# Kernel optimization log

Hardware: AMD Instinct MI355X
Metric: run time of the kernel (lower is better)

## Reference

```python
import math
import jax, jax.numpy as jnp
import numpy as np


def setup_inputs() -> dict:
    key = jax.random.key(0)
    k1, k2 = jax.random.split(key)
    x = jax.random.normal(k1, (32, 3, 64, 64), dtype=jnp.float32)   # (B,C,H,W)
    y = jax.random.normal(k2, (512, 3, 64, 64), dtype=jnp.float32)  # (N,C,H,W)
    return {"x": x, "y": y}


def reference(x, y):
    # Faithful to torch rfft/irfft with normalized=True (unitary / 'ortho' scaling).
    B, C, H, W = x.shape
    scale = math.sqrt(H * W)  # self.N in the torch module
    X = jnp.fft.rfft2(x, norm="ortho")  # (B,C,H,W//2+1) complex
    Y = jnp.fft.rfft2(y, norm="ortho")  # (N,C,H,W//2+1) complex
    # conj(X) . Y summed over channels, fused as one complex contraction
    G = jnp.einsum("bchw,nchw->bnhw", jnp.conj(X), Y)  # (B,N,H,W//2+1)
    g = jnp.fft.irfft2(G, s=(H, W), norm="ortho") * scale  # (B,N,H,W)
    m = jnp.max(g, axis=(-2, -1))  # MaxPool2d(kernel=input_size) -> (B,N)
    xx = jnp.linalg.norm(x.reshape(B, -1), axis=-1)[:, None]  # (B,1)
    yy = jnp.linalg.norm(y.reshape(y.shape[0], -1), axis=-1)[None, :]  # (1,N)
    return m / xx / yy
```

## Files before the change

### kernel.cpp

```cpp
#include <hip/hip_runtime.h>
#include <math.h>

#define FBINS 2112
#define CSC 66

typedef float cplx __attribute__((ext_vector_type(2)));
typedef __fp16 half2v __attribute__((ext_vector_type(2)));
#define MK2(a,b) (cplx){(float)(a), (float)(b)}

__device__ __forceinline__ cplx shufxy(cplx a){ return __builtin_shufflevector(a, a, 1, 0); }
template<int S> __device__ __forceinline__ cplx imul(cplx a){
    return (S > 0) ? shufxy(a) * MK2(-1.f, 1.f) : shufxy(a) * MK2(1.f, -1.f);
}
template<int S> __device__ __forceinline__ cplx cmul_tw(cplx a, cplx w){
    cplx ws = shufxy(w);
    return (S > 0) ? a.x*w + a.y*(ws*MK2(-1.f, 1.f))
                   : a.x*(w*MK2(1.f, -1.f)) + a.y*ws;
}

__device__ __forceinline__ unsigned pack16(float a, float b){
    half2v h = __builtin_amdgcn_cvt_pkrtz(a, b);
    return __builtin_bit_cast(unsigned, h);
}
__device__ __forceinline__ half2v h2(unsigned u){ return __builtin_bit_cast(half2v, u); }
__device__ __forceinline__ float fdot2(half2v a, half2v b, float c){
#if __has_builtin(__builtin_amdgcn_fdot2)
    return __builtin_amdgcn_fdot2(a, b, c, false);
#else
    return c + (float)a.x*(float)b.x + (float)a.y*(float)b.y;
#endif
}
__device__ __forceinline__ void dotw(unsigned ux, unsigned uy, float& r, float& s){
    unsigned ys = ((uy >> 16) | (uy << 16)) ^ 0x80000000u;
    r = fdot2(h2(ux), h2(uy), r);
    s = fdot2(h2(ux), h2(ys), s);
}
__device__ __forceinline__ void dotw_i(unsigned ux, unsigned uy, cplx& v){
    float rr = 0.f, ss = 0.f;
    dotw(ux, uy, rr, ss);
    v += MK2(-ss, rr);
}

__device__ __constant__ float TWC[112] = {
  1.f,0.f, 1.f,0.f, 1.f,0.f, 1.f,0.f, 1.f,0.f, 1.f,0.f, 1.f,0.f,
  0.9951847267f,0.0980171403f, 0.9807852804f,0.1950903220f, 0.9569403357f,0.2902846773f,
  0.9238795325f,0.3826834324f, 0.8819212643f,0.4713967368f, 0.8314696123f,0.5555702330f,
  0.7730104534f,0.6343932842f,
  0.9807852804f,0.1950903220f, 0.9238795325f,0.3826834324f, 0.8314696123f,0.5555702330f,
  0.7071067812f,0.7071067812f, 0.5555702330f,0.8314696123f, 0.3826834324f,0.9238795325f,
  0.1950903220f,0.9807852804f,
  0.9569403357f,0.2902846773f, 0.8314696123f,0.5555702330f, 0.6343932842f,0.7730104534f,
  0.3826834324f,0.9238795325f, 0.0980171403f,0.9951847267f, -0.1950903220f,0.9807852804f,
  -0.4713967368f,0.8819212643f,
  0.9238795325f,0.3826834324f, 0.7071067812f,0.7071067812f, 0.3826834324f,0.9238795325f,
  0.f,1.f, -0.3826834324f,0.9238795325f, -0.7071067812f,0.7071067812f,
  -0.9238795325f,0.3826834324f,
  0.8819212643f,0.4713967368f, 0.5555702330f,0.8314696123f, 0.0980171403f,0.9951847267f,
  -0.3826834324f,0.9238795325f, -0.7730104534f,0.6343932842f, -0.9807852804f,0.1950903220f,
  -0.9569403357f,-0.2902846773f,
  0.8314696123f,0.5555702330f, 0.3826834324f,0.9238795325f, -0.1950903220f,0.9807852804f,
  -0.7071067812f,0.7071067812f, -0.9807852804f,0.1950903220f, -0.9238795325f,-0.3826834324f,
  -0.5555702330f,-0.8314696123f,
  0.7730104534f,0.6343932842f, 0.1950903220f,0.9807852804f, -0.4713967368f,0.8819212643f,
  -0.9238795325f,0.3826834324f, -0.9569403357f,-0.2902846773f, -0.5555702330f,-0.8314696123f,
  0.0980171403f,-0.9951847267f
};
__device__ __forceinline__ void load_tw(int j, cplx wj[7]){
    #pragma unroll
    for (int k=0;k<7;++k) wj[k] = MK2(TWC[(j*7+k)*2], TWC[(j*7+k)*2+1]);
}

template<int S>
__device__ __forceinline__ void dft8(cplx v[8]) {
    const float C = 0.70710678118654752440f;
    cplx t0=v[0]+v[4], t4=v[0]-v[4];
    cplx t1=v[1]+v[5], t5=v[1]-v[5];
    cplx t2=v[2]+v[6], t6=v[2]-v[6];
    cplx t3=v[3]+v[7], t7=v[3]-v[7];
    cplx u0=t0+t2, u2=t0-t2;
    cplx u1=t1+t3, u3=t1-t3;
    v[0]=u0+u1; v[4]=u0-u1;
    cplx m3=imul<S>(u3);
    v[2]=u2+m3; v[6]=u2-m3;
    cplx z0=t4;
    cplx z1 = C*(t5 + imul<S>(t5));
    cplx z2 = imul<S>(t6);
    cplx z3 = C*(imul<S>(t7) - t7);
    cplx w0=z0+z2, w2=z0-z2;
    cplx w1=z1+z3, w3=z1-z3;
    v[1]=w0+w1; v[5]=w0-w1;
    cplx mb=imul<S>(w3);
    v[3]=w2+mb; v[7]=w2-mb;
}

template<int S>
__device__ __forceinline__ void fft64_from_regs(
    cplx v[8], cplx* __restrict__ mem, int base, int j, const cplx wj[7])
{
    dft8<S>(v);
    #pragma unroll
    for (int k=1;k<8;++k) v[k] = cmul_tw<S>(v[k], wj[k-1]);
    #pragma unroll
    for (int k=0;k<8;++k) mem[base + 8*j + (k^j)] = v[k];
    #pragma unroll
    for (int n=0;n<8;++n) v[n] = mem[base + 8*n + (j^n)];
    dft8<S>(v);
}

__global__ __launch_bounds__(256) void fwd_fft_kernel(
    const float* __restrict__ in, unsigned* __restrict__ o,
    float* __restrict__ pn)
{
    __shared__ __align__(16) cplx CL[2176];
    __shared__ float red[4];
    const int tid = threadIdx.x, G = tid>>3, j = tid&7;

    cplx wj[7]; load_tw(j, wj);
    const float* img = in + (size_t)blockIdx.x * 4096;

    {
        cplx v[8];
        float ns = 0.f;
        #pragma unroll
        for (int nn=0;nn<8;++nn){ int w=8*nn+j;
            float a = img[64*G + w], c = img[64*(G+32) + w];
            v[nn] = MK2(a, c);
            ns = fmaf(a, a, ns); ns = fmaf(c, c, ns); }
        #pragma unroll
        for (int off = 32; off; off >>= 1) ns += __shfl_xor(ns, off);
        if ((tid & 63) == 0) red[tid >> 6] = ns;
        int base = CSC*G;
        fft64_from_regs<-1>(v, CL, base, j, wj);
        #pragma unroll
        for (int k=0;k<8;++k) CL[base + j + 8*k] = v[k];
    }
    __syncthreads();

    {
        cplx v[8];
        if (G == 0) {
            #pragma unroll
            for (int nn=0;nn<8;++nn){
                int r=8*nn+j, p=r&31, hi=r>>5;
                cplx a0  = CL[CSC*p + 0];
                cplx a32 = CL[CSC*p + 32];
                v[nn] = hi ? MK2(a0.y, a32.y) : MK2(a0.x, a32.x);
            }
        } else {
            const int c = G;
            #pragma unroll
            for (int nn=0;nn<8;++nn){
                int r=8*nn+j, p=r&31, hi=r>>5;
                cplx A  = CL[CSC*p + c];
                cplx Bm = CL[CSC*p + 64 - c];
                if (!hi) v[nn] = 0.5f*(A + Bm*MK2(1.f,-1.f));
                else     v[nn] = 0.5f*(shufxy(A)*MK2(1.f,-1.f) + shufxy(Bm));
            }
        }
        __syncthreads();
        int base = CSC*G;
        fft64_from_regs<-1>(v, CL, base, j, wj);
        #pragma unroll
        for (int k=0;k<8;++k) CL[base + j + 8*k] = v[k];
    }
    __syncthreads();

    unsigned* a = o + (size_t)blockIdx.x * FBINS;
    for (int i = tid; i < FBINS; i += 256) {
        int wp = i>>6, h = i&63;
        cplx r;
        if (wp == 0) {
            int h2i = (64-h)&63;
            cplx av = CL[h], bb = CL[h2i];
            r = 0.5f*(av + bb*MK2(1.f,-1.f));
        } else if (wp == 32) {
            int h2i = (64-h)&63;
            cplx av = CL[h], bb = CL[h2i];
            r = 0.5f*(shufxy(av)*MK2(1.f,-1.f) + shufxy(bb));
        } else {
            r = CL[CSC*wp + h];
        }
        int slot = ((h & 7) << 3) | (h >> 3);
        a[(wp << 6) | slot] = pack16(r.x, r.y);
    }
    if (tid == 0) pn[blockIdx.x] = red[0] + red[1] + red[2] + red[3];
}

__global__ __launch_bounds__(256) void corr_kernel(
    const unsigned* __restrict__ Xh, const unsigned* __restrict__ Yh,
    const float* __restrict__ px, const float* __restrict__ py,
    float* __restrict__ out)
{
    __shared__ __align__(16) cplx CL[2176];
    __shared__ float red[4];
    const int tid = threadIdx.x, G = tid>>3, j = tid&7;

    const int blk = blockIdx.x;
    const int xcd = blk & 7, idx = blk >> 3;
    const int n = xcd*64 + (idx & 63);
    const int b = idx >> 6;

    const float x2 = px[3*b] + px[3*b+1] + px[3*b+2];
    const float y2 = py[3*n] + py[3*n+1] + py[3*n+2];
    const float dinv = rsqrtf(x2 * y2) * (1.0f/4096.0f);

    const uint4* pX4 = (const uint4*)Xh + (size_t)b * 3 * 528;
    const uint4* pY4 = (const uint4*)Yh + (size_t)n * 3 * 528;
    cplx v[8];
    {
        float r[8], s[8];
        #pragma unroll
        for (int k=0;k<8;++k){ r[k]=0.f; s[k]=0.f; }
        const int off = 16*G + 2*j;
        #pragma unroll
        for (int ch = 0; ch < 3; ++ch) {
            uint4 x0 = pX4[ch*528 + off], x1 = pX4[ch*528 + off + 1];
            uint4 y0 = pY4[ch*528 + off], y1 = pY4[ch*528 + off + 1];
            dotw(x0.x, y0.x, r[0], s[0]);  dotw(x0.y, y0.y, r[1], s[1]);
            dotw(x0.z, y0.z, r[2], s[2]);  dotw(x0.w, y0.w, r[3], s[3]);
            dotw(x1.x, y1.x, r[4], s[4]);  dotw(x1.y, y1.y, r[5], s[5]);
            dotw(x1.z, y1.z, r[6], s[6]);  dotw(x1.w, y1.w, r[7], s[7]);
        }
        #pragma unroll
        for (int k=0;k<8;++k) v[k] = MK2(r[k], s[k]);
    }
    if (G == 0) {
        const int off = 512 + 2*j;
        #pragma unroll
        for (int ch = 0; ch < 3; ++ch) {
            uint4 x0 = pX4[ch*528 + off], x1 = pX4[ch*528 + off + 1];
            uint4 y0 = pY4[ch*528 + off], y1 = pY4[ch*528 + off + 1];
            dotw_i(x0.x, y0.x, v[0]);  dotw_i(x0.y, y0.y, v[1]);
            dotw_i(x0.z, y0.z, v[2]);  dotw_i(x0.w, y0.w, v[3]);
            dotw_i(x1.x, y1.x, v[4]);  dotw_i(x1.y, y1.y, v[5]);
            dotw_i(x1.z, y1.z, v[6]);  dotw_i(x1.w, y1.w, v[7]);
        }
    }

    cplx wj[7]; load_tw(j, wj);

    fft64_from_regs<1>(v, CL, CSC*G, j, wj);
    #pragma unroll
    for (int k=0;k<4;++k)
        *(float4*)&CL[CSC*G + 2*(j+8*k)] =
            make_float4(v[k].x, v[k].y, v[k+4].x, v[k+4].y);
    __syncthreads();

    float m = -3.4e38f;
    {
        if (j == 0) {
            float4 f = *(float4*)&CL[2*G];
            v[0] = MK2(f.x, f.z);
            v[4] = MK2(f.y, f.w);
        } else {
            float4 f = *(float4*)&CL[CSC*j + 2*G];
            v[0] = MK2(f.x,f.y) + imul<1>(MK2(f.z,f.w));
            float4 g2 = *(float4*)&CL[CSC*(32-j) + 2*G];
            v[4] = MK2(g2.x,g2.y)*MK2(1.f,-1.f) + shufxy(MK2(g2.z,g2.w));
        }
        #pragma unroll
        for (int nn=1;nn<4;++nn){
            int w = 8*nn + j;
            float4 f = *(float4*)&CL[CSC*w + 2*G];
            v[nn] = MK2(f.x,f.y) + imul<1>(MK2(f.z,f.w));
        }
        #pragma unroll
        for (int nn=5;nn<8;++nn){
            int w2 = 64 - (8*nn + j);
            float4 f = *(float4*)&CL[CSC*w2 + 2*G];
            v[nn] = MK2(f.x,f.y)*MK2(1.f,-1.f) + shufxy(MK2(f.z,f.w));
        }
        __syncthreads();
        fft64_from_regs<1>(v, CL, CSC*G, j, wj);
        #pragma unroll
        for (int k=0;k<8;++k) m = fmaxf(m, fmaxf(v[k].x, v[k].y));
    }
    #pragma unroll
    for (int off = 32; off; off >>= 1) m = fmaxf(m, __shfl_xor(m, off));
    if ((tid & 63) == 0) red[tid >> 6] = m;
    __syncthreads();
    if (tid == 0) {
        float mm = fmaxf(fmaxf(red[0], red[1]), fmaxf(red[2], red[3]));
        out[b*512 + n] = mm * dinv;
    }
}

extern "C" void kernel_launch(void* const* d_in, const int* in_sizes, int n_in,
                              void* d_out, int out_size, void* d_ws, size_t ws_size,
                              hipStream_t stream) {
    const float* x = (const float*)d_in[0];
    const float* y = (const float*)d_in[1];
    float* out = (float*)d_out;

    unsigned* Xh = (unsigned*)d_ws;
    unsigned* Yh = Xh + 96 * FBINS;
    float* px = (float*)(Yh + 1536 * FBINS);
    float* py = px + 96;

    fwd_fft_kernel<<<96,   256, 0, stream>>>(x, Xh, px);
    fwd_fft_kernel<<<1536, 256, 0, stream>>>(y, Yh, py);
    corr_kernel<<<16384, 256, 0, stream>>>(Xh, Yh, px, py, out);
}
```

Baseline: 83.53 us.

## Fuse X/Y forward FFT launches and precompute swapped X spectra for correlation

The two forward FFT launches become one 1632-block launch that selects the x or y image per block. X spectra are now written twice, once plain and once pre-rotated (conjugate/swap form, with special handling of the Nyquist column), so the correlation kernel's inner loop needs no per-element half-swap and sign flip before the second dot. The Nyquist-row handling is folded into the same accumulators, and the shared-memory transpose addresses are precomputed into arrays. This adds an extra X buffer and one more global load stream per channel in the hot correlation loop.

```diff
diff --git a/kernel.cpp b/kernel.cpp
--- a/kernel.cpp
+++ b/kernel.cpp
@@ -29,16 +29,6 @@
 #else
     return c + (float)a.x*(float)b.x + (float)a.y*(float)b.y;
 #endif
-}
-__device__ __forceinline__ void dotw(unsigned ux, unsigned uy, float& r, float& s){
-    unsigned ys = ((uy >> 16) | (uy << 16)) ^ 0x80000000u;
-    r = fdot2(h2(ux), h2(uy), r);
-    s = fdot2(h2(ux), h2(ys), s);
-}
-__device__ __forceinline__ void dotw_i(unsigned ux, unsigned uy, cplx& v){
-    float rr = 0.f, ss = 0.f;
-    dotw(ux, uy, rr, ss);
-    v += MK2(-ss, rr);
 }
 
 __device__ __constant__ float TWC[112] = {
@@ -95,28 +85,42 @@
 
 template<int S>
 __device__ __forceinline__ void fft64_from_regs(
-    cplx v[8], cplx* __restrict__ mem, int base, int j, const cplx wj[7])
+    cplx v[8], cplx* __restrict__ mem, const int wa[8], const int ra[8],
+    const cplx wj[7])
 {
     dft8<S>(v);
     #pragma unroll
     for (int k=1;k<8;++k) v[k] = cmul_tw<S>(v[k], wj[k-1]);
     #pragma unroll
-    for (int k=0;k<8;++k) mem[base + 8*j + (k^j)] = v[k];
-    #pragma unroll
-    for (int n=0;n<8;++n) v[n] = mem[base + 8*n + (j^n)];
+    for (int k=0;k<8;++k) mem[wa[k]] = v[k];
+    #pragma unroll
+    for (int n=0;n<8;++n) v[n] = mem[ra[n]];
     dft8<S>(v);
 }
 
 __global__ __launch_bounds__(256) void fwd_fft_kernel(
-    const float* __restrict__ in, unsigned* __restrict__ o,
-    float* __restrict__ pn)
+    const float* __restrict__ x, const float* __restrict__ y,
+    unsigned* __restrict__ Xa, unsigned* __restrict__ Xb,
+    unsigned* __restrict__ Yh, float* __restrict__ pn)
 {
     __shared__ __align__(16) cplx CL[2176];
     __shared__ float red[4];
     const int tid = threadIdx.x, G = tid>>3, j = tid&7;
+    const int blk = blockIdx.x;
+    const bool isX = blk < 96;
 
     cplx wj[7]; load_tw(j, wj);
-    const float* img = in + (size_t)blockIdx.x * 4096;
+    int wa[8], ra[8];
+    {
+        int base = CSC*G;
+        #pragma unroll
+        for (int k=0;k<8;++k) wa[k] = base + 8*j + (k^j);
+        #pragma unroll
+        for (int k=0;k<8;++k) ra[k] = base + 8*k + (j^k);
+    }
+
+    const float* img = (isX ? x + (size_t)blk * 4096
+                            : y + (size_t)(blk - 96) * 4096);
 
     {
         cplx v[8];
@@ -129,8 +133,8 @@
         #pragma unroll
         for (int off = 32; off; off >>= 1) ns += __shfl_xor(ns, off);
         if ((tid & 63) == 0) red[tid >> 6] = ns;
+        fft64_from_regs<-1>(v, CL, wa, ra, wj);
         int base = CSC*G;
-        fft64_from_regs<-1>(v, CL, base, j, wj);
         #pragma unroll
         for (int k=0;k<8;++k) CL[base + j + 8*k] = v[k];
     }
@@ -158,14 +162,13 @@
             }
         }
         __syncthreads();
+        fft64_from_regs<-1>(v, CL, wa, ra, wj);
         int base = CSC*G;
-        fft64_from_regs<-1>(v, CL, base, j, wj);
         #pragma unroll
         for (int k=0;k<8;++k) CL[base + j + 8*k] = v[k];
     }
     __syncthreads();
 
-    unsigned* a = o + (size_t)blockIdx.x * FBINS;
     for (int i = tid; i < FBINS; i += 256) {
         int wp = i>>6, h = i&63;
         cplx r;
@@ -180,14 +183,21 @@
         } else {
             r = CL[CSC*wp + h];
         }
-        int slot = ((h & 7) << 3) | (h >> 3);
-        a[(wp << 6) | slot] = pack16(r.x, r.y);
-    }
-    if (tid == 0) pn[blockIdx.x] = red[0] + red[1] + red[2] + red[3];
+        int slot = (wp << 6) | ((h & 7) << 3) | (h >> 3);
+        if (isX) {
+            size_t o = (size_t)blk * FBINS + slot;
+            if (wp == 32) { Xa[o] = pack16(r.y, -r.x); Xb[o] = pack16(r.x, r.y); }
+            else          { Xa[o] = pack16(r.x, r.y);  Xb[o] = pack16(-r.y, r.x); }
+        } else {
+            Yh[(size_t)(blk - 96) * FBINS + slot] = pack16(r.x, r.y);
+        }
+    }
+    if (tid == 0) pn[blk] = red[0] + red[1] + red[2] + red[3];
 }
 
 __global__ __launch_bounds__(256) void corr_kernel(
-    const unsigned* __restrict__ Xh, const unsigned* __restrict__ Yh,
+    const unsigned* __restrict__ Xa, const unsigned* __restrict__ Xb,
+    const unsigned* __restrict__ Yh,
     const float* __restrict__ px, const float* __restrict__ py,
     float* __restrict__ out)
 {
@@ -204,8 +214,18 @@
     const float y2 = py[3*n] + py[3*n+1] + py[3*n+2];
     const float dinv = rsqrtf(x2 * y2) * (1.0f/4096.0f);
 
-    const uint4* pX4 = (const uint4*)Xh + (size_t)b * 3 * 528;
-    const uint4* pY4 = (const uint4*)Yh + (size_t)n * 3 * 528;
+    int wa[8], ra[8];
+    {
+        int base = CSC*G;
+        #pragma unroll
+        for (int k=0;k<8;++k) wa[k] = base + 8*j + (k^j);
+        #pragma unroll
+        for (int k=0;k<8;++k) ra[k] = base + 8*k + (j^k);
+    }
+
+    const uint4* pXa = (const uint4*)Xa + (size_t)b * 3 * 528;
+    const uint4* pXb = (const uint4*)Xb + (size_t)b * 3 * 528;
+    const uint4* pY  = (const uint4*)Yh + (size_t)n * 3 * 528;
     cplx v[8];
     {
         float r[8], s[8];
@@ -214,32 +234,42 @@
         const int off = 16*G + 2*j;
         #pragma unroll
         for (int ch = 0; ch < 3; ++ch) {
-            uint4 x0 = pX4[ch*528 + off], x1 = pX4[ch*528 + off + 1];
-            uint4 y0 = pY4[ch*528 + off], y1 = pY4[ch*528 + off + 1];
-            dotw(x0.x, y0.x, r[0], s[0]);  dotw(x0.y, y0.y, r[1], s[1]);
-            dotw(x0.z, y0.z, r[2], s[2]);  dotw(x0.w, y0.w, r[3], s[3]);
-            dotw(x1.x, y1.x, r[4], s[4]);  dotw(x1.y, y1.y, r[5], s[5]);
-            dotw(x1.z, y1.z, r[6], s[6]);  dotw(x1.w, y1.w, r[7], s[7]);
+            uint4 a0 = pXa[ch*528 + off], a1 = pXa[ch*528 + off + 1];
+            uint4 b0 = pXb[ch*528 + off], b1 = pXb[ch*528 + off + 1];
+            uint4 y0 = pY [ch*528 + off], y1 = pY [ch*528 + off + 1];
+            r[0]=fdot2(h2(a0.x),h2(y0.x),r[0]); s[0]=fdot2(h2(b0.x),h2(y0.x),s[0]);
+            r[1]=fdot2(h2(a0.y),h2(y0.y),r[1]); s[1]=fdot2(h2(b0.y),h2(y0.y),s[1]);
+            r[2]=fdot2(h2(a0.z),h2(y0.z),r[2]); s[2]=fdot2(h2(b0.z),h2(y0.z),s[2]);
+            r[3]=fdot2(h2(a0.w),h2(y0.w),r[3]); s[3]=fdot2(h2(b0.w),h2(y0.w),s[3]);
+            r[4]=fdot2(h2(a1.x),h2(y1.x),r[4]); s[4]=fdot2(h2(b1.x),h2(y1.x),s[4]);
+            r[5]=fdot2(h2(a1.y),h2(y1.y),r[5]); s[5]=fdot2(h2(b1.y),h2(y1.y),s[5]);
+            r[6]=fdot2(h2(a1.z),h2(y1.z),r[6]); s[6]=fdot2(h2(b1.z),h2(y1.z),s[6]);
+            r[7]=fdot2(h2(a1.w),h2(y1.w),r[7]); s[7]=fdot2(h2(b1.w),h2(y1.w),s[7]);
+        }
+        if (G == 0) {
+            const int off2 = 512 + 2*j;
+            #pragma unroll
+            for (int ch = 0; ch < 3; ++ch) {
+                uint4 a0 = pXa[ch*528 + off2], a1 = pXa[ch*528 + off2 + 1];
+                uint4 b0 = pXb[ch*528 + off2], b1 = pXb[ch*528 + off2 + 1];
+                uint4 y0 = pY [ch*528 + off2], y1 = pY [ch*528 + off2 + 1];
+                r[0]=fdot2(h2(a0.x),h2(y0.x),r[0]); s[0]=fdot2(h2(b0.x),h2(y0.x),s[0]);
+                r[1]=fdot2(h2(a0.y),h2(y0.y),r[1]); s[1]=fdot2(h2(b0.y),h2(y0.y),s[1]);
+                r[2]=fdot2(h2(a0.z),h2(y0.z),r[2]); s[2]=fdot2(h2(b0.z),h2(y0.z),s[2]);
+                r[3]=fdot2(h2(a0.w),h2(y0.w),r[3]); s[3]=fdot2(h2(b0.w),h2(y0.w),s[3]);
+                r[4]=fdot2(h2(a1.x),h2(y1.x),r[4]); s[4]=fdot2(h2(b1.x),h2(y1.x),s[4]);
+                r[5]=fdot2(h2(a1.y),h2(y1.y),r[5]); s[5]=fdot2(h2(b1.y),h2(y1.y),s[5]);
+                r[6]=fdot2(h2(a1.z),h2(y1.z),r[6]); s[6]=fdot2(h2(b1.z),h2(y1.z),s[6]);
+                r[7]=fdot2(h2(a1.w),h2(y1.w),r[7]); s[7]=fdot2(h2(b1.w),h2(y1.w),s[7]);
+            }
         }
         #pragma unroll
         for (int k=0;k<8;++k) v[k] = MK2(r[k], s[k]);
     }
-    if (G == 0) {
-        const int off = 512 + 2*j;
-        #pragma unroll
-        for (int ch = 0; ch < 3; ++ch) {
-            uint4 x0 = pX4[ch*528 + off], x1 = pX4[ch*528 + off + 1];
-            uint4 y0 = pY4[ch*528 + off], y1 = pY4[ch*528 + off + 1];
-            dotw_i(x0.x, y0.x, v[0]);  dotw_i(x0.y, y0.y, v[1]);
-            dotw_i(x0.z, y0.z, v[2]);  dotw_i(x0.w, y0.w, v[3]);
-            dotw_i(x1.x, y1.x, v[4]);  dotw_i(x1.y, y1.y, v[5]);
-            dotw_i(x1.z, y1.z, v[6]);  dotw_i(x1.w, y1.w, v[7]);
-        }
-    }
 
     cplx wj[7]; load_tw(j, wj);
 
-    fft64_from_regs<1>(v, CL, CSC*G, j, wj);
+    fft64_from_regs<1>(v, CL, wa, ra, wj);
     #pragma unroll
     for (int k=0;k<4;++k)
         *(float4*)&CL[CSC*G + 2*(j+8*k)] =
@@ -271,7 +301,7 @@
             v[nn] = MK2(f.x,f.y)*MK2(1.f,-1.f) + shufxy(MK2(f.z,f.w));
         }
         __syncthreads();
-        fft64_from_regs<1>(v, CL, CSC*G, j, wj);
+        fft64_from_regs<1>(v, CL, wa, ra, wj);
         #pragma unroll
         for (int k=0;k<8;++k) m = fmaxf(m, fmaxf(v[k].x, v[k].y));
     }
@@ -292,12 +322,13 @@
     const float* y = (const float*)d_in[1];
     float* out = (float*)d_out;
 
-    unsigned* Xh = (unsigned*)d_ws;
-    unsigned* Yh = Xh + 96 * FBINS;
-    float* px = (float*)(Yh + 1536 * FBINS);
-    float* py = px + 96;
-
-    fwd_fft_kernel<<<96,   256, 0, stream>>>(x, Xh, px);
-    fwd_fft_kernel<<<1536, 256, 0, stream>>>(y, Yh, py);
-    corr_kernel<<<16384, 256, 0, stream>>>(Xh, Yh, px, py, out);
-}
+    unsigned* Xa = (unsigned*)d_ws;
+    unsigned* Xb = Xa + 96 * FBINS;
+    unsigned* Yh = Xb + 96 * FBINS;
+    float* pn = (float*)(Yh + 1536 * FBINS);
+    float* px = pn;
+    float* py = pn + 96;
+
+    fwd_fft_kernel<<<1632, 256, 0, stream>>>(x, y, Xa, Xb, Yh, pn);
+    corr_kernel<<<16384, 256, 0, stream>>>(Xa, Xb, Yh, px, py, out);
+}
```

Result: slower. 90.87 us (+8.8%).
